# Performance work log

Hardware: AMD Instinct MI355X
Metric: run time of the kernel (lower is better)

The kernel has to match this reference:

```python
import jax, jax.numpy as jnp
import numpy as np

HEADS = 16
DIM = 64  # per-head dim
SCALE = DIM ** (-0.5)


def setup_inputs() -> dict:
    key = jax.random.key(0)
    k1, k2, k3 = jax.random.split(key, 3)
    B, T, E = 2, 2048, 1024
    x = jax.random.normal(k1, (B, T, E), dtype=jnp.float32)
    # torch Linear weights are [out_features, in_features]; init std=0.02
    w_qkv = jax.random.normal(k2, (3 * DIM * HEADS, E), dtype=jnp.float32) * 0.02
    w_out = jax.random.normal(k3, (E, DIM * HEADS), dtype=jnp.float32) * 0.02
    return {"x": x, "w_qkv": w_qkv, "w_out": w_out}


def reference(x, w_qkv, w_out):
    B, T, E = x.shape
    qkv = jnp.einsum('bte,fe->btf', x, w_qkv)  # [B, T, 3*DIM*HEADS]
    # einops 'b t (k d h) -> k b h t d': last dim splits as (k, d, h) with h fastest
    qkv = qkv.reshape(B, T, 3, DIM, HEADS).transpose(2, 0, 4, 1, 3)  # [3, B, H, T, D]
    q, k, v = qkv[0], qkv[1], qkv[2]
    dots = jnp.einsum('bhid,bhjd->bhij', q, k) * SCALE  # [B, H, T, T]
    attn = jax.nn.softmax(dots, axis=-1)
    out = jnp.einsum('bhij,bhjd->bhid', attn, v)  # [B, H, T, D]
    # 'b h t d -> b t (h d)'
    out = out.transpose(0, 2, 1, 3).reshape(B, T, HEADS * DIM)
    return jnp.einsum('btf,ef->bte', out, w_out)  # [B, T, E]
```

## Files before the change

kernel.cpp:

```cpp
#include <hip/hip_runtime.h>
#include <hip/hip_bf16.h>
#include <stdint.h>


using u16 = uint16_t;
typedef __bf16 bf16x8 __attribute__((ext_vector_type(8)));
typedef float f32x4 __attribute__((ext_vector_type(4)));
typedef float f32x16 __attribute__((ext_vector_type(16)));
typedef unsigned short ushort8 __attribute__((ext_vector_type(8)));
typedef uint32_t u32x4 __attribute__((ext_vector_type(4)));
typedef unsigned int u32x2v __attribute__((ext_vector_type(2)));

#define DEV __device__ __forceinline__

typedef __attribute__((address_space(1))) void as1_void;
typedef __attribute__((address_space(3))) void as3_void;

DEV void async16(void* lds_uniform, const void* gsrc) {
    __builtin_amdgcn_global_load_lds((as1_void*)(gsrc), (as3_void*)(lds_uniform), 16, 0, 0);
}

DEV uint16_t f2bf(float x) {
    uint32_t u = __builtin_bit_cast(uint32_t, x);
    u += 0x7fffu + ((u >> 16) & 1u);
    return (uint16_t)(u >> 16);
}

DEV uint32_t pack2(float a, float b) {
    return (uint32_t)f2bf(a) | ((uint32_t)f2bf(b) << 16);
}

DEV uint32_t cvtpk(float lo, float hi) {
    uint32_t r;
    asm("v_cvt_pk_bf16_f32 %0, %1, %2" : "=v"(r) : "v"(lo), "v"(hi));
    return r;
}

DEV float exp2r(float x) { return __builtin_amdgcn_exp2f(x); }

__global__ __launch_bounds__(256) void k_cvt3(const float* __restrict__ x,
                                              const float* __restrict__ wq,
                                              const float* __restrict__ wo,
                                              u16* __restrict__ xb,
                                              u16* __restrict__ wqb,
                                              u16* __restrict__ wob) {
    int i = blockIdx.x * 256 + threadIdx.x;
    const float* in;
    u16* out;
    int j;
    if (i < 524288)       { in = x;  out = xb;  j = i; }
    else if (i < 917504)  { in = wq; out = wqb; j = i - 524288; }
    else                  { in = wo; out = wob; j = i - 917504; }
    const float4* p = (const float4*)in;
    float4 a = p[2 * (size_t)j], b = p[2 * (size_t)j + 1];
    ushort8 o;
    o[0] = f2bf(a.x); o[1] = f2bf(a.y); o[2] = f2bf(a.z); o[3] = f2bf(a.w);
    o[4] = f2bf(b.x); o[5] = f2bf(b.y); o[6] = f2bf(b.z); o[7] = f2bf(b.w);
    *(ushort8*)(out + 8 * (size_t)j) = o;
}


struct QFrag { bf16x8 a[4][2]; bf16x8 b[2][2]; };

template <int MG, int NG>
DEV void qkv_read(const char* lds, int vA0, int vA1, int vB0, int vB1, int cb, QFrag& f) {
#pragma unroll
    for (int i = 0; i < 4; ++i) {
        f.a[i][0] = *(const bf16x8*)(lds + cb + vA0 + (MG * 4 + i) * 2048);
        f.a[i][1] = *(const bf16x8*)(lds + cb + vA1 + (MG * 4 + i) * 2048);
    }
#pragma unroll
    for (int j = 0; j < 2; ++j) {
        f.b[j][0] = *(const bf16x8*)(lds + cb + vB0 + (NG * 2 + j) * 2048);
        f.b[j][1] = *(const bf16x8*)(lds + cb + vB1 + (NG * 2 + j) * 2048);
    }
}

template <int MG, int NG>
DEV void qkv_mma(const QFrag& f, f32x4 (&acc)[8][4]) {
    __builtin_amdgcn_s_setprio(1);
#pragma unroll
    for (int i = 0; i < 4; ++i)
#pragma unroll
        for (int j = 0; j < 2; ++j)
#pragma unroll
            for (int kk = 0; kk < 2; ++kk)
                acc[MG * 4 + i][NG * 2 + j] = __builtin_amdgcn_mfma_f32_16x16x32_bf16(
                    f.a[i][kk], f.b[j][kk], acc[MG * 4 + i][NG * 2 + j], 0, 0, 0);
    __builtin_amdgcn_s_setprio(0);
}

__global__ __launch_bounds__(512) void k_gemm_qkv(const u16* __restrict__ A,
                                                  const u16* __restrict__ B,
                                                  u16* __restrict__ Qp,
                                                  u16* __restrict__ Kp,
                                                  u16* __restrict__ Vtp) {
    __shared__ __align__(16) char smem[131072];
    const int tid = threadIdx.x;
    const int lane = tid & 63, wid = tid >> 6;
    const int r = lane & 15, g = lane >> 4;
    const int wm = wid >> 2, wn = wid & 3;
    const int lin = blockIdx.x;
    const int wg = (lin & 7) * 24 + (lin >> 3);
    const int m0 = (wg / 12) * 256, n0 = (wg % 12) * 256;

    f32x4 acc[8][4] = {};

    const int colswz = ((g ^ (r & 7)) << 4);
    const int vA0 = wm * 16384 + r * 128 + colswz;
    const int vA1 = vA0 ^ 64;
    const int vB0 = 65536 + (wn >> 1) * 16384 + ((wn & 1) * 64 + r) * 128 + colswz;
    const int vB1 = vB0 ^ 64;
    const char* ldsR = (const char*)smem;

    const int lr = tid >> 3;
    const int scol = (((tid & 7) * 16) ^ ((lr & 7) << 4)) >> 1;
    const u16* aS = A + (size_t)(m0 + lr) * 1024 + scol;
    const u16* bS = B + (size_t)(n0 + lr) * 1024 + scol;
    char* ldsT = (char*)smem + tid * 16;

    auto STAGE = [&](int region, const u16* src) {
        async16(ldsT + region,        src);
        async16(ldsT + region + 8192, src + 64 * 1024);
    };

    STAGE(0,              aS);
    STAGE(16384,          aS + 131072);
    STAGE(65536,          bS);
    STAGE(65536 + 16384,  bS + 131072);

    for (int t = 0; t < 16; ++t) {
        const int cb = (t & 1) << 15;
        const int nb = ((t + 1) & 1) << 15;
        const u16* aN = aS + (t + 1) * 64;
        const u16* bN = bS + (t + 1) * 64;
        QFrag f;

        if (t < 15) {
            STAGE(nb, aN);
            asm volatile("s_waitcnt vmcnt(2)" ::: "memory");
        } else {
            asm volatile("s_waitcnt vmcnt(0)" ::: "memory");
        }
        __builtin_amdgcn_s_barrier();
        asm volatile("" ::: "memory");
        qkv_read<0, 0>(ldsR, vA0, vA1, vB0, vB1, cb, f);
        qkv_mma<0, 0>(f, acc);
        __builtin_amdgcn_s_barrier();
        asm volatile("" ::: "memory");

        qkv_read<0, 1>(ldsR, vA0, vA1, vB0, vB1, cb, f);
        if (t < 15) STAGE(nb + 16384, aN + 131072);
        __builtin_amdgcn_s_barrier();
        asm volatile("" ::: "memory");
        qkv_mma<0, 1>(f, acc);
        __builtin_amdgcn_s_barrier();
        asm volatile("" ::: "memory");

        qkv_read<1, 0>(ldsR, vA0, vA1, vB0, vB1, cb, f);
        if (t < 15) STAGE(nb + 65536, bN);
        __builtin_amdgcn_s_barrier();
        asm volatile("" ::: "memory");
        qkv_mma<1, 0>(f, acc);
        __builtin_amdgcn_s_barrier();
        asm volatile("" ::: "memory");

        qkv_read<1, 1>(ldsR, vA0, vA1, vB0, vB1, cb, f);
        if (t < 15) STAGE(nb + 65536 + 16384, bN + 131072);
        __builtin_amdgcn_s_barrier();
        asm volatile("" ::: "memory");
        qkv_mma<1, 1>(f, acc);
        __builtin_amdgcn_s_barrier();
        asm volatile("" ::: "memory");
    }

    const int fbase = n0 + wn * 64;
    const int which = fbase >> 10;
    const int dbase = (fbase & 1023) >> 4;
    if (which < 2) {
        u16* P = which ? Kp : Qp;
#pragma unroll
        for (int m = 0; m < 8; ++m) {
#pragma unroll
            for (int reg = 0; reg < 4; ++reg) {
                int tt = m0 + wm * 128 + m * 16 + g * 4 + reg;
                int b = tt >> 11, t = tt & 2047;
                u16* dst = P + (((size_t)(b * 16 + r) * 2048 + t) * 64 + dbase);
                uint2 val;
                val.x = pack2(acc[m][0][reg], acc[m][1][reg]);
                val.y = pack2(acc[m][2][reg], acc[m][3][reg]);
                *(uint2*)dst = val;
            }
        }
    } else {
#pragma unroll
        for (int m = 0; m < 8; ++m) {
            int tt0 = m0 + wm * 128 + m * 16 + g * 4;
            int b = tt0 >> 11, t0 = tt0 & 2047;
#pragma unroll
            for (int n = 0; n < 4; ++n) {
                u16* dst = Vtp + (((size_t)(b * 16 + r) * 64 + dbase + n) * 2048 + t0);
                uint2 val;
                val.x = pack2(acc[m][n][0], acc[m][n][1]);
                val.y = pack2(acc[m][n][2], acc[m][n][3]);
                *(uint2*)dst = val;
            }
        }
    }
}

__global__ __launch_bounds__(256) void k_gemm_out(const u16* __restrict__ A,
                                                  const u16* __restrict__ B,
                                                  float* __restrict__ C) {
    constexpr int N = 1024, K = 1024, BK = 32;
    __shared__ u16 As[128 * BK];
    __shared__ u16 Bs[128 * BK];
    const int tid = threadIdx.x;
    const int lane = tid & 63, wv = tid >> 6;
    const int g = lane >> 4, r = lane & 15;
    const int lin = blockIdx.x;
    const int wg = (lin & 7) * 32 + (lin >> 3);
    const int m0 = (wg >> 3) * 128, n0 = (wg & 7) * 128;
    const int wr = (wv >> 1) * 64, wc = (wv & 1) * 64;

    f32x4 acc[4][4] = {};

    const int row0 = (tid * 16) >> 6;
    const int cole = ((tid * 16) & 63) >> 1;
    const u16* ga0 = A + (size_t)(m0 + row0) * K + cole;
    const u16* ga1 = A + (size_t)(m0 + 64 + row0) * K + cole;
    const u16* gb0 = B + (size_t)(n0 + row0) * K + cole;
    const u16* gb1 = B + (size_t)(n0 + 64 + row0) * K + cole;
    char* lA = (char*)As + wv * 1024;
    char* lB = (char*)Bs + wv * 1024;

    for (int k0 = 0; k0 < K; k0 += BK) {
        async16(lA,        ga0 + k0);
        async16(lA + 4096, ga1 + k0);
        async16(lB,        gb0 + k0);
        async16(lB + 4096, gb1 + k0);
        __syncthreads();

        bf16x8 af[4], bfr[4];
#pragma unroll
        for (int m = 0; m < 4; ++m)
            af[m] = *(const bf16x8*)&As[(wr + m * 16 + r) * BK + g * 8];
#pragma unroll
        for (int n = 0; n < 4; ++n)
            bfr[n] = *(const bf16x8*)&Bs[(wc + n * 16 + r) * BK + g * 8];
#pragma unroll
        for (int m = 0; m < 4; ++m)
#pragma unroll
            for (int n = 0; n < 4; ++n)
                acc[m][n] = __builtin_amdgcn_mfma_f32_16x16x32_bf16(af[m], bfr[n], acc[m][n], 0, 0, 0);
        __syncthreads();
    }

#pragma unroll
    for (int m = 0; m < 4; ++m) {
#pragma unroll
        for (int reg = 0; reg < 4; ++reg) {
            size_t crow = (size_t)(m0 + wr + m * 16 + g * 4 + reg);
#pragma unroll
            for (int n = 0; n < 4; ++n)
                C[crow * N + n0 + wc + n * 16 + r] = acc[m][n][reg];
        }
    }
}

__global__ __launch_bounds__(512, 1) void k_attn(const u16* __restrict__ Qp,
                                                 const u16* __restrict__ Kp,
                                                 const u16* __restrict__ Vtp,
                                                 u16* __restrict__ O) {
    constexpr int T = 2048;
    constexpr float ALPHA = 0.18033688f;
    __shared__ __align__(16) char smem[65536];

    const int tid = threadIdx.x;
    const int lane = tid & 63, wv = tid >> 6;
    const int l31 = lane & 31, hi = lane >> 5;

    const int lin = blockIdx.x;
    const int work = (lin & 7) * 32 + (lin >> 3);
    const int bh = work >> 3, qchunk = work & 7;
    const int q0 = qchunk * 256 + wv * 32;

    const u16* Qb = Qp + (size_t)bh * T * 64;
    const u16* Kb = Kp + (size_t)bh * T * 64;
    const u16* Vb = Vtp + (size_t)bh * 64 * T;

    const u16* qrow = Qb + (size_t)(q0 + l31) * 64 + hi * 8;
    bf16x8 qf[4];
#pragma unroll
    for (int kb = 0; kb < 4; ++kb) qf[kb] = *(const bf16x8*)(qrow + kb * 16);

    const char* ldsB = (const char*)smem;
    int off[4];
#pragma unroll
    for (int s = 0; s < 4; ++s)
        off[s] = l31 * 128 + ((((2 * s + hi) ^ (l31 & 7))) << 4);

    const int srow = tid >> 3;
    const int scol = (((tid & 7) * 16) ^ ((srow & 7) << 4)) >> 1;
    const u16* kSrc = Kb + srow * 64 + scol;
    const u16* vSrc = Vb + (size_t)srow * T + scol;
    char* ldsT = smem + tid * 16;

    f32x16 st[2], pex[2], oa[2];
    f32x16 z;
#pragma unroll
    for (int e = 0; e < 16; ++e) { z[e] = 0.f; oa[0][e] = 0.f; oa[1][e] = 0.f; }
    bf16x8 pf[4] = {};
    float lrow = 0.f;

    async16(ldsT, kSrc);
    async16(ldsT + 32768, vSrc);

    for (int it4 = 0; it4 < 8; ++it4) {
#pragma unroll
        for (int sub = 0; sub < 4; ++sub) {
            const int it = it4 * 4 + sub;
            const int KB = sub * 8192;
            const int VBprev = 32768 + ((sub + 3) & 3) * 8192;
            const int KBnext = ((sub + 1) & 3) * 8192;
            const int VBnext = 32768 + ((sub + 1) & 3) * 8192;

            if (it != 31) {
                async16(ldsT + KBnext, kSrc + (size_t)(it + 1) * 4096);
                async16(ldsT + VBnext, vSrc + (it + 1) * 64);
                asm volatile("s_waitcnt vmcnt(3)" ::: "memory");
            } else {
                asm volatile("s_waitcnt vmcnt(0)" ::: "memory");
            }
            __builtin_amdgcn_s_barrier();
            asm volatile("" ::: "memory");

            __builtin_amdgcn_s_setprio(1);
            {
                bf16x8 k0 = *(const bf16x8*)(ldsB + off[0] + KB);
                bf16x8 k1 = *(const bf16x8*)(ldsB + off[0] + KB + 4096);
                st[0] = __builtin_amdgcn_mfma_f32_32x32x16_bf16(k0, qf[0], z, 0, 0, 0);
                st[1] = __builtin_amdgcn_mfma_f32_32x32x16_bf16(k1, qf[0], z, 0, 0, 0);
            }
#pragma unroll
            for (int kb = 1; kb < 4; ++kb) {
                bf16x8 k0 = *(const bf16x8*)(ldsB + off[kb] + KB);
                bf16x8 k1 = *(const bf16x8*)(ldsB + off[kb] + KB + 4096);
                st[0] = __builtin_amdgcn_mfma_f32_32x32x16_bf16(k0, qf[kb], st[0], 0, 0, 0);
                st[1] = __builtin_amdgcn_mfma_f32_32x32x16_bf16(k1, qf[kb], st[1], 0, 0, 0);
            }
            if (it4 + sub != 0) {
#pragma unroll
                for (int jk = 0; jk < 4; ++jk) {
                    bf16x8 v0 = *(const bf16x8*)(ldsB + off[jk] + VBprev);
                    bf16x8 v1 = *(const bf16x8*)(ldsB + off[jk] + VBprev + 4096);
                    oa[0] = __builtin_amdgcn_mfma_f32_32x32x16_bf16(v0, pf[jk], oa[0], 0, 0, 0);
                    oa[1] = __builtin_amdgcn_mfma_f32_32x32x16_bf16(v1, pf[jk], oa[1], 0, 0, 0);
                }
            }
            __builtin_amdgcn_s_setprio(0);

#pragma unroll
            for (int tt = 0; tt < 2; ++tt)
#pragma unroll
                for (int e = 0; e < 16; ++e)
                    pex[tt][e] = exp2r(st[tt][e] * ALPHA);

            float ps0 = 0.f, ps1 = 0.f;
#pragma unroll
            for (int e = 0; e < 16; e += 2) { ps0 += pex[0][e]; ps1 += pex[0][e + 1]; }
#pragma unroll
            for (int e = 0; e < 16; e += 2) { ps0 += pex[1][e]; ps1 += pex[1][e + 1]; }
            lrow += ps0 + ps1;

#pragma unroll
            for (int t = 0; t < 2; ++t) {
                uint32_t c0 = cvtpk(pex[t][0], pex[t][1]);
                uint32_t c1 = cvtpk(pex[t][2], pex[t][3]);
                uint32_t c2 = cvtpk(pex[t][4], pex[t][5]);
                uint32_t c3 = cvtpk(pex[t][6], pex[t][7]);
                uint32_t c4 = cvtpk(pex[t][8], pex[t][9]);
                uint32_t c5 = cvtpk(pex[t][10], pex[t][11]);
                uint32_t c6 = cvtpk(pex[t][12], pex[t][13]);
                uint32_t c7 = cvtpk(pex[t][14], pex[t][15]);
                u32x2v s0 = __builtin_amdgcn_permlane32_swap(c0, c2, false, false);
                u32x2v s1 = __builtin_amdgcn_permlane32_swap(c1, c3, false, false);
                u32x2v s2 = __builtin_amdgcn_permlane32_swap(c4, c6, false, false);
                u32x2v s3 = __builtin_amdgcn_permlane32_swap(c5, c7, false, false);
                u32x4 f0; f0.x = s0[0]; f0.y = s1[0]; f0.z = s0[1]; f0.w = s1[1];
                u32x4 f1; f1.x = s2[0]; f1.y = s3[0]; f1.z = s2[1]; f1.w = s3[1];
                pf[2 * t]     = __builtin_bit_cast(bf16x8, f0);
                pf[2 * t + 1] = __builtin_bit_cast(bf16x8, f1);
            }

            asm volatile("" ::: "memory");
        }
    }

#pragma unroll
    for (int jk = 0; jk < 4; ++jk) {
        bf16x8 v0 = *(const bf16x8*)(ldsB + off[jk] + 57344);
        bf16x8 v1 = *(const bf16x8*)(ldsB + off[jk] + 57344 + 4096);
        oa[0] = __builtin_amdgcn_mfma_f32_32x32x16_bf16(v0, pf[jk], oa[0], 0, 0, 0);
        oa[1] = __builtin_amdgcn_mfma_f32_32x32x16_bf16(v1, pf[jk], oa[1], 0, 0, 0);
    }

    lrow += __shfl_xor(lrow, 32);
    float linv = 1.0f / lrow;
    const int b = bh >> 4, h = bh & 15;
    u16* obase = O + ((size_t)b * T + q0 + l31) * 1024 + h * 64 + 4 * hi;
#pragma unroll
    for (int q = 0; q < 8; ++q) {
        int dbase = ((2 * q) & 3) + 8 * (q >> 1);
        *(uint32_t*)(obase + dbase)      = pack2(oa[0][2 * q] * linv, oa[0][2 * q + 1] * linv);
        *(uint32_t*)(obase + 32 + dbase) = pack2(oa[1][2 * q] * linv, oa[1][2 * q + 1] * linv);
    }
}

extern "C" void kernel_launch(void* const* d_in, const int* in_sizes, int n_in,
                              void* d_out, int out_size, void* d_ws, size_t ws_size,
                              hipStream_t stream) {
    const float* x    = (const float*)d_in[0];
    const float* wqkv = (const float*)d_in[1];
    const float* wout = (const float*)d_in[2];
    float* out = (float*)d_out;
    char* ws = (char*)d_ws;

    u16* xb   = (u16*)(ws);
    u16* wqb  = (u16*)(ws + 8388608);
    u16* wob  = (u16*)(ws + 14680064);
    u16* Qp   = (u16*)(ws + 41943040);
    u16* Kp   = (u16*)(ws + 50331648);
    u16* Vtp  = (u16*)(ws + 58720256);
    u16* Ob   = (u16*)(ws + 67108864);

    k_cvt3<<<4096, 256, 0, stream>>>(x, wqkv, wout, xb, wqb, wob);
    k_gemm_qkv<<<dim3(192), 512, 0, stream>>>(xb, wqb, Qp, Kp, Vtp);
    k_attn<<<dim3(256), dim3(512), 0, stream>>>(Qp, Kp, Vtp, Ob);
    k_gemm_out<<<dim3(256), 256, 0, stream>>>(Ob, wob, out);
}
```

Before: 121.8 us.

## Retile QKV GEMM to 256x192 for 256 blocks and pipeline output GEMM

The QKV projection GEMM moves from 256x256 tiles (192 blocks) to 256x192 tiles (256 blocks), which better fills the 256 CUs. Its sub-phased barrier schedule becomes a single-stage double-buffered loop with one barrier pair per k-step. The output GEMM is rewritten to 512 threads with swizzled LDS, 64-wide k-steps and async double buffering in place of the unpipelined BK=32 loop. This trades the finer-grained overlap of the old QKV kernel for more parallelism and fewer barriers, and each wave in the QKV kernel now holds a 4x6 accumulator tile.

```diff
diff --git a/kernel.cpp b/kernel.cpp
--- a/kernel.cpp
+++ b/kernel.cpp
@@ -59,59 +59,153 @@
     *(ushort8*)(out + 8 * (size_t)j) = o;
 }
 
-
-struct QFrag { bf16x8 a[4][2]; bf16x8 b[2][2]; };
-
-template <int MG, int NG>
-DEV void qkv_read(const char* lds, int vA0, int vA1, int vB0, int vB1, int cb, QFrag& f) {
-#pragma unroll
-    for (int i = 0; i < 4; ++i) {
-        f.a[i][0] = *(const bf16x8*)(lds + cb + vA0 + (MG * 4 + i) * 2048);
-        f.a[i][1] = *(const bf16x8*)(lds + cb + vA1 + (MG * 4 + i) * 2048);
-    }
-#pragma unroll
-    for (int j = 0; j < 2; ++j) {
-        f.b[j][0] = *(const bf16x8*)(lds + cb + vB0 + (NG * 2 + j) * 2048);
-        f.b[j][1] = *(const bf16x8*)(lds + cb + vB1 + (NG * 2 + j) * 2048);
-    }
-}
-
-template <int MG, int NG>
-DEV void qkv_mma(const QFrag& f, f32x4 (&acc)[8][4]) {
-    __builtin_amdgcn_s_setprio(1);
-#pragma unroll
-    for (int i = 0; i < 4; ++i)
-#pragma unroll
-        for (int j = 0; j < 2; ++j)
-#pragma unroll
-            for (int kk = 0; kk < 2; ++kk)
-                acc[MG * 4 + i][NG * 2 + j] = __builtin_amdgcn_mfma_f32_16x16x32_bf16(
-                    f.a[i][kk], f.b[j][kk], acc[MG * 4 + i][NG * 2 + j], 0, 0, 0);
-    __builtin_amdgcn_s_setprio(0);
-}
-
 __global__ __launch_bounds__(512) void k_gemm_qkv(const u16* __restrict__ A,
                                                   const u16* __restrict__ B,
                                                   u16* __restrict__ Qp,
                                                   u16* __restrict__ Kp,
                                                   u16* __restrict__ Vtp) {
-    __shared__ __align__(16) char smem[131072];
+    __shared__ __align__(16) char smem[114688];
+    const int tid = threadIdx.x;
+    const int lane = tid & 63, wid = tid >> 6;
+    const int r = lane & 15, g = lane >> 4;
+    const int wm = wid >> 1, wn = wid & 1;
+    const int lin = blockIdx.x;
+    const int wg = (lin & 7) * 32 + (lin >> 3);
+    const int m0 = (wg >> 4) * 256, n0 = (wg & 15) * 192;
+
+    f32x4 acc[4][6] = {};
+
+    const int colswz = (g ^ (r & 7)) << 4;
+    int vA[4], vB[6];
+#pragma unroll
+    for (int m = 0; m < 4; ++m)
+        vA[m] = wm * 8192 + (m * 16 + r) * 128 + colswz;
+#pragma unroll
+    for (int j = 0; j < 6; ++j) {
+        int jj = wn * 96 + j * 16 + r;
+        vB[j] = 65536 + (jj >> 6) * 8192 + (jj & 63) * 128 + colswz;
+    }
+    const char* lds = (const char*)smem;
+
+    const int lr = tid >> 3;
+    const int scol = (((tid & 7) * 16) ^ ((lr & 7) << 4)) >> 1;
+    const u16* aS = A + (size_t)(m0 + lr) * 1024 + scol;
+    const u16* bS = B + (size_t)(n0 + lr) * 1024 + scol;
+    char* ldsT = (char*)smem + tid * 16;
+
+    auto STAGE_ALL = [&](int buf, int t) {
+        const u16* a = aS + t * 64;
+        const u16* b = bS + t * 64;
+        char* dA = ldsT + buf * 32768;
+        char* dB = ldsT + 65536 + buf * 24576;
+        async16(dA,          a);
+        async16(dA + 8192,   a + 65536);
+        async16(dA + 16384,  a + 131072);
+        async16(dA + 24576,  a + 196608);
+        async16(dB,          b);
+        async16(dB + 8192,   b + 65536);
+        async16(dB + 16384,  b + 131072);
+    };
+
+    STAGE_ALL(0, 0);
+
+    for (int t = 0; t < 16; ++t) {
+        const int buf = t & 1;
+        if (t < 15) {
+            STAGE_ALL(buf ^ 1, t + 1);
+            asm volatile("s_waitcnt vmcnt(7)" ::: "memory");
+        } else {
+            asm volatile("s_waitcnt vmcnt(0)" ::: "memory");
+        }
+        __builtin_amdgcn_s_barrier();
+        asm volatile("" ::: "memory");
+
+        bf16x8 a[4][2];
+#pragma unroll
+        for (int m = 0; m < 4; ++m) {
+            int ad = buf * 32768 + vA[m];
+            a[m][0] = *(const bf16x8*)(lds + ad);
+            a[m][1] = *(const bf16x8*)(lds + (ad ^ 64));
+        }
+        __builtin_amdgcn_s_setprio(1);
+#pragma unroll
+        for (int j = 0; j < 6; ++j) {
+            int bd = buf * 24576 + vB[j];
+            bf16x8 b0 = *(const bf16x8*)(lds + bd);
+            bf16x8 b1 = *(const bf16x8*)(lds + (bd ^ 64));
+#pragma unroll
+            for (int m = 0; m < 4; ++m) {
+                acc[m][j] = __builtin_amdgcn_mfma_f32_16x16x32_bf16(a[m][0], b0, acc[m][j], 0, 0, 0);
+                acc[m][j] = __builtin_amdgcn_mfma_f32_16x16x32_bf16(a[m][1], b1, acc[m][j], 0, 0, 0);
+            }
+        }
+        __builtin_amdgcn_s_setprio(0);
+        asm volatile("s_waitcnt lgkmcnt(0)" ::: "memory");
+        __builtin_amdgcn_s_barrier();
+        asm volatile("" ::: "memory");
+    }
+
+#pragma unroll
+    for (int jp = 0; jp < 3; ++jp) {
+        const int f0 = n0 + wn * 96 + jp * 32;
+        const int which = f0 >> 10;
+        const int d0 = (f0 & 1023) >> 4;
+        if (which < 2) {
+            u16* P = which ? Kp : Qp;
+#pragma unroll
+            for (int m = 0; m < 4; ++m) {
+#pragma unroll
+                for (int reg = 0; reg < 4; ++reg) {
+                    int tt = m0 + wm * 64 + m * 16 + g * 4 + reg;
+                    int b = tt >> 11, t = tt & 2047;
+                    *(uint32_t*)(P + (((size_t)(b * 16 + r) * 2048 + t) * 64 + d0))
+                        = pack2(acc[m][2 * jp][reg], acc[m][2 * jp + 1][reg]);
+                }
+            }
+        } else {
+#pragma unroll
+            for (int m = 0; m < 4; ++m) {
+                int tt0 = m0 + wm * 64 + m * 16 + g * 4;
+                int b = tt0 >> 11, t0 = tt0 & 2047;
+#pragma unroll
+                for (int dj = 0; dj < 2; ++dj) {
+                    uint2 val;
+                    val.x = pack2(acc[m][2 * jp + dj][0], acc[m][2 * jp + dj][1]);
+                    val.y = pack2(acc[m][2 * jp + dj][2], acc[m][2 * jp + dj][3]);
+                    *(uint2*)(Vtp + (((size_t)(b * 16 + r) * 64 + d0 + dj) * 2048 + t0)) = val;
+                }
+            }
+        }
+    }
+}
+
+__global__ __launch_bounds__(512) void k_gemm_out(const u16* __restrict__ A,
+                                                  const u16* __restrict__ B,
+                                                  float* __restrict__ C) {
+    __shared__ __align__(16) char smem[65536];
     const int tid = threadIdx.x;
     const int lane = tid & 63, wid = tid >> 6;
     const int r = lane & 15, g = lane >> 4;
     const int wm = wid >> 2, wn = wid & 3;
     const int lin = blockIdx.x;
-    const int wg = (lin & 7) * 24 + (lin >> 3);
-    const int m0 = (wg / 12) * 256, n0 = (wg % 12) * 256;
-
-    f32x4 acc[8][4] = {};
-
-    const int colswz = ((g ^ (r & 7)) << 4);
-    const int vA0 = wm * 16384 + r * 128 + colswz;
-    const int vA1 = vA0 ^ 64;
-    const int vB0 = 65536 + (wn >> 1) * 16384 + ((wn & 1) * 64 + r) * 128 + colswz;
-    const int vB1 = vB0 ^ 64;
-    const char* ldsR = (const char*)smem;
+    const int wg = (lin & 7) * 32 + (lin >> 3);
+    const int m0 = (wg >> 3) * 128, n0 = (wg & 7) * 128;
+
+    f32x4 acc[4][2] = {};
+
+    const int colswz = (g ^ (r & 7)) << 4;
+    int vA[4], vB[2];
+#pragma unroll
+    for (int m = 0; m < 4; ++m) {
+        int ii = wm * 64 + m * 16 + r;
+        vA[m] = (ii >> 6) * 8192 + (ii & 63) * 128 + colswz;
+    }
+#pragma unroll
+    for (int n = 0; n < 2; ++n) {
+        int jj = wn * 32 + n * 16 + r;
+        vB[n] = 32768 + (jj >> 6) * 8192 + (jj & 63) * 128 + colswz;
+    }
+    const char* lds = (const char*)smem;
 
     const int lr = tid >> 3;
     const int scol = (((tid & 7) * 16) ^ ((lr & 7) << 4)) >> 1;
@@ -119,151 +213,63 @@
     const u16* bS = B + (size_t)(n0 + lr) * 1024 + scol;
     char* ldsT = (char*)smem + tid * 16;
 
-    auto STAGE = [&](int region, const u16* src) {
-        async16(ldsT + region,        src);
-        async16(ldsT + region + 8192, src + 64 * 1024);
+    auto STAGE_ALL = [&](int buf, int t) {
+        const u16* a = aS + t * 64;
+        const u16* b = bS + t * 64;
+        async16(ldsT + buf * 16384,          a);
+        async16(ldsT + buf * 16384 + 8192,   a + 65536);
+        async16(ldsT + 32768 + buf * 16384,        b);
+        async16(ldsT + 32768 + buf * 16384 + 8192, b + 65536);
     };
 
-    STAGE(0,              aS);
-    STAGE(16384,          aS + 131072);
-    STAGE(65536,          bS);
-    STAGE(65536 + 16384,  bS + 131072);
+    STAGE_ALL(0, 0);
 
     for (int t = 0; t < 16; ++t) {
-        const int cb = (t & 1) << 15;
-        const int nb = ((t + 1) & 1) << 15;
-        const u16* aN = aS + (t + 1) * 64;
-        const u16* bN = bS + (t + 1) * 64;
-        QFrag f;
-
+        const int buf = t & 1;
         if (t < 15) {
-            STAGE(nb, aN);
-            asm volatile("s_waitcnt vmcnt(2)" ::: "memory");
+            STAGE_ALL(buf ^ 1, t + 1);
+            asm volatile("s_waitcnt vmcnt(4)" ::: "memory");
         } else {
             asm volatile("s_waitcnt vmcnt(0)" ::: "memory");
         }
         __builtin_amdgcn_s_barrier();
         asm volatile("" ::: "memory");
-        qkv_read<0, 0>(ldsR, vA0, vA1, vB0, vB1, cb, f);
-        qkv_mma<0, 0>(f, acc);
+
+        bf16x8 a[4][2], b[2][2];
+#pragma unroll
+        for (int m = 0; m < 4; ++m) {
+            int ad = buf * 16384 + vA[m];
+            a[m][0] = *(const bf16x8*)(lds + ad);
+            a[m][1] = *(const bf16x8*)(lds + (ad ^ 64));
+        }
+#pragma unroll
+        for (int n = 0; n < 2; ++n) {
+            int bd = buf * 16384 + vB[n];
+            b[n][0] = *(const bf16x8*)(lds + bd);
+            b[n][1] = *(const bf16x8*)(lds + (bd ^ 64));
+        }
+        __builtin_amdgcn_s_setprio(1);
+#pragma unroll
+        for (int m = 0; m < 4; ++m)
+#pragma unroll
+            for (int n = 0; n < 2; ++n) {
+                acc[m][n] = __builtin_amdgcn_mfma_f32_16x16x32_bf16(a[m][0], b[n][0], acc[m][n], 0, 0, 0);
+                acc[m][n] = __builtin_amdgcn_mfma_f32_16x16x32_bf16(a[m][1], b[n][1], acc[m][n], 0, 0, 0);
+            }
+        __builtin_amdgcn_s_setprio(0);
+        asm volatile("s_waitcnt lgkmcnt(0)" ::: "memory");
         __builtin_amdgcn_s_barrier();
         asm volatile("" ::: "memory");
-
-        qkv_read<0, 1>(ldsR, vA0, vA1, vB0, vB1, cb, f);
-        if (t < 15) STAGE(nb + 16384, aN + 131072);
-        __builtin_amdgcn_s_barrier();
-        asm volatile("" ::: "memory");
-        qkv_mma<0, 1>(f, acc);
-        __builtin_amdgcn_s_barrier();
-        asm volatile("" ::: "memory");
-
-        qkv_read<1, 0>(ldsR, vA0, vA1, vB0, vB1, cb, f);
-        if (t < 15) STAGE(nb + 65536, bN);
-        __builtin_amdgcn_s_barrier();
-        asm volatile("" ::: "memory");
-        qkv_mma<1, 0>(f, acc);
-        __builtin_amdgcn_s_barrier();
-        asm volatile("" ::: "memory");
-
-        qkv_read<1, 1>(ldsR, vA0, vA1, vB0, vB1, cb, f);
-        if (t < 15) STAGE(nb + 65536 + 16384, bN + 131072);
-        __builtin_amdgcn_s_barrier();
-        asm volatile("" ::: "memory");
-        qkv_mma<1, 1>(f, acc);
-        __builtin_amdgcn_s_barrier();
-        asm volatile("" ::: "memory");
-    }
-
-    const int fbase = n0 + wn * 64;
-    const int which = fbase >> 10;
-    const int dbase = (fbase & 1023) >> 4;
-    if (which < 2) {
-        u16* P = which ? Kp : Qp;
-#pragma unroll
-        for (int m = 0; m < 8; ++m) {
-#pragma unroll
-            for (int reg = 0; reg < 4; ++reg) {
-                int tt = m0 + wm * 128 + m * 16 + g * 4 + reg;
-                int b = tt >> 11, t = tt & 2047;
-                u16* dst = P + (((size_t)(b * 16 + r) * 2048 + t) * 64 + dbase);
-                uint2 val;
-                val.x = pack2(acc[m][0][reg], acc[m][1][reg]);
-                val.y = pack2(acc[m][2][reg], acc[m][3][reg]);
-                *(uint2*)dst = val;
-            }
-        }
-    } else {
-#pragma unroll
-        for (int m = 0; m < 8; ++m) {
-            int tt0 = m0 + wm * 128 + m * 16 + g * 4;
-            int b = tt0 >> 11, t0 = tt0 & 2047;
-#pragma unroll
-            for (int n = 0; n < 4; ++n) {
-                u16* dst = Vtp + (((size_t)(b * 16 + r) * 64 + dbase + n) * 2048 + t0);
-                uint2 val;
-                val.x = pack2(acc[m][n][0], acc[m][n][1]);
-                val.y = pack2(acc[m][n][2], acc[m][n][3]);
-                *(uint2*)dst = val;
-            }
-        }
-    }
-}
-
-__global__ __launch_bounds__(256) void k_gemm_out(const u16* __restrict__ A,
-                                                  const u16* __restrict__ B,
-                                                  float* __restrict__ C) {
-    constexpr int N = 1024, K = 1024, BK = 32;
-    __shared__ u16 As[128 * BK];
-    __shared__ u16 Bs[128 * BK];
-    const int tid = threadIdx.x;
-    const int lane = tid & 63, wv = tid >> 6;
-    const int g = lane >> 4, r = lane & 15;
-    const int lin = blockIdx.x;
-    const int wg = (lin & 7) * 32 + (lin >> 3);
-    const int m0 = (wg >> 3) * 128, n0 = (wg & 7) * 128;
-    const int wr = (wv >> 1) * 64, wc = (wv & 1) * 64;
-
-    f32x4 acc[4][4] = {};
-
-    const int row0 = (tid * 16) >> 6;
-    const int cole = ((tid * 16) & 63) >> 1;
-    const u16* ga0 = A + (size_t)(m0 + row0) * K + cole;
-    const u16* ga1 = A + (size_t)(m0 + 64 + row0) * K + cole;
-    const u16* gb0 = B + (size_t)(n0 + row0) * K + cole;
-    const u16* gb1 = B + (size_t)(n0 + 64 + row0) * K + cole;
-    char* lA = (char*)As + wv * 1024;
-    char* lB = (char*)Bs + wv * 1024;
-
-    for (int k0 = 0; k0 < K; k0 += BK) {
-        async16(lA,        ga0 + k0);
-        async16(lA + 4096, ga1 + k0);
-        async16(lB,        gb0 + k0);
-        async16(lB + 4096, gb1 + k0);
-        __syncthreads();
-
-        bf16x8 af[4], bfr[4];
-#pragma unroll
-        for (int m = 0; m < 4; ++m)
-            af[m] = *(const bf16x8*)&As[(wr + m * 16 + r) * BK + g * 8];
-#pragma unroll
-        for (int n = 0; n < 4; ++n)
-            bfr[n] = *(const bf16x8*)&Bs[(wc + n * 16 + r) * BK + g * 8];
-#pragma unroll
-        for (int m = 0; m < 4; ++m)
-#pragma unroll
-            for (int n = 0; n < 4; ++n)
-                acc[m][n] = __builtin_amdgcn_mfma_f32_16x16x32_bf16(af[m], bfr[n], acc[m][n], 0, 0, 0);
-        __syncthreads();
     }
 
 #pragma unroll
     for (int m = 0; m < 4; ++m) {
 #pragma unroll
         for (int reg = 0; reg < 4; ++reg) {
-            size_t crow = (size_t)(m0 + wr + m * 16 + g * 4 + reg);
-#pragma unroll
-            for (int n = 0; n < 4; ++n)
-                C[crow * N + n0 + wc + n * 16 + r] = acc[m][n][reg];
+            size_t crow = (size_t)(m0 + wm * 64 + m * 16 + g * 4 + reg);
+#pragma unroll
+            for (int n = 0; n < 2; ++n)
+                C[crow * 1024 + n0 + wn * 32 + n * 16 + r] = acc[m][n][reg];
         }
     }
 }
@@ -435,7 +441,7 @@
     u16* Ob   = (u16*)(ws + 67108864);
 
     k_cvt3<<<4096, 256, 0, stream>>>(x, wqkv, wout, xb, wqb, wob);
-    k_gemm_qkv<<<dim3(192), 512, 0, stream>>>(xb, wqb, Qp, Kp, Vtp);
+    k_gemm_qkv<<<dim3(256), 512, 0, stream>>>(xb, wqb, Qp, Kp, Vtp);
     k_attn<<<dim3(256), dim3(512), 0, stream>>>(Qp, Kp, Vtp, Ob);
-    k_gemm_out<<<dim3(256), 256, 0, stream>>>(Ob, wob, out);
-}
+    k_gemm_out<<<dim3(256), 512, 0, stream>>>(Ob, wob, out);
+}
```

Measured after the change: 117.5 us. -3.6%, faster.
